# Kernel optimization log

Measured on AMD Instinct MI355X. Metric: run time of the kernel, lower is better.

Reference implementation:

```python
import jax, jax.numpy as jnp
import numpy as np
import math

B, L, D, H = 2, 2048, 1024, 16
DH = D // H  # 64


def setup_inputs() -> dict:
    key = jax.random.key(0)
    ks = jax.random.split(key, 8)
    s = 1.0 / math.sqrt(D)
    return {
        "query": jax.random.normal(ks[0], (B, L, D), dtype=jnp.float32),
        "key": jax.random.normal(ks[1], (B, L, D), dtype=jnp.float32),
        "value": jax.random.normal(ks[2], (B, L, D), dtype=jnp.float32),
        "attn_mask": jax.random.bernoulli(ks[3], 0.1, (B, L, L)),  # True = masked
        "Wq": jax.random.normal(ks[4], (D, D), dtype=jnp.float32) * s,
        "Wk": jax.random.normal(ks[5], (D, D), dtype=jnp.float32) * s,
        "Wv": jax.random.normal(ks[6], (D, D), dtype=jnp.float32) * s,
        "Wo": jax.random.normal(ks[7], (D, D), dtype=jnp.float32) * s,
    }


def reference(query, key, value, attn_mask, Wq, Wk, Wv, Wo):
    # torch nn.Linear computes x @ W.T (bias=False here)
    def shape(x):
        b, l, _ = x.shape
        return x.reshape(b, l, H, DH).transpose(0, 2, 1, 3)  # [B,H,L,DH]

    q = shape(query @ Wq.T) / jnp.sqrt(jnp.float32(DH))
    k = shape(key @ Wk.T)
    v = shape(value @ Wv.T)

    scores = jnp.einsum("bhqd,bhkd->bhqk", q, k)  # [B,H,Q,K]
    if attn_mask is not None:
        scores = jnp.where(attn_mask[:, None, :, :], jnp.float32(-1e18), scores)
    attn = jax.nn.softmax(scores, axis=-1)
    # dropout p=0.0 (eval/deterministic) -> identity
    context = jnp.einsum("bhqk,bhkd->bhqd", attn, v)
    context = context.transpose(0, 2, 1, 3).reshape(query.shape[0], -1, D)
    output = context @ Wo.T
    top_attn = attn[:, 0, :, :]
    return output, top_attn
```

## Files before the change

### kernel.cpp

```cpp
#include <hip/hip_runtime.h>

#define BB 2
#define LL 2048
#define DD 1024
#define HH 16
#define DHH 64

typedef _Float16 f16;
typedef _Float16 f16x8 __attribute__((ext_vector_type(8)));
typedef _Float16 f16x4 __attribute__((ext_vector_type(4)));
typedef _Float16 f16x2 __attribute__((ext_vector_type(2)));
typedef float f32x4 __attribute__((ext_vector_type(4)));
typedef unsigned long long u64;

#define VWAIT(N) asm volatile("s_waitcnt vmcnt(" #N ")" ::: "memory")
#define LWAIT0() asm volatile("s_waitcnt lgkmcnt(0)" ::: "memory")
#define SB0() __builtin_amdgcn_sched_barrier(0)

__device__ __forceinline__ void gload_lds16(const void* g, void* l) {
    __builtin_amdgcn_global_load_lds(
        (const __attribute__((address_space(1))) void*)g,
        (__attribute__((address_space(3))) void*)l, 16, 0, 0);
}

__device__ __forceinline__ f16x4 cvt4f(float4 v) {
    f16x4 o;
    o[0] = (f16)v.x; o[1] = (f16)v.y; o[2] = (f16)v.z; o[3] = (f16)v.w;
    return o;
}

__device__ __forceinline__ f16x8 cvt8f(float4 a, float4 b) {
    f16x2 p0 = __builtin_bit_cast(f16x2, __builtin_amdgcn_cvt_pkrtz(a.x, a.y));
    f16x2 p1 = __builtin_bit_cast(f16x2, __builtin_amdgcn_cvt_pkrtz(a.z, a.w));
    f16x2 p2 = __builtin_bit_cast(f16x2, __builtin_amdgcn_cvt_pkrtz(b.x, b.y));
    f16x2 p3 = __builtin_bit_cast(f16x2, __builtin_amdgcn_cvt_pkrtz(b.z, b.w));
    f16x8 r;
    r[0] = p0[0]; r[1] = p0[1]; r[2] = p1[0]; r[3] = p1[1];
    r[4] = p2[0]; r[5] = p2[1]; r[6] = p3[0]; r[7] = p3[1];
    return r;
}

__global__ void prep(const int* __restrict__ msk,
                     const float* __restrict__ wq, const float* __restrict__ wk,
                     const float* __restrict__ wv, const float* __restrict__ wo,
                     f16* __restrict__ wh, u64* __restrict__ Mp) {
    const int tid = threadIdx.x;
    if (blockIdx.y == 0) {
        const int lane = tid & 63;
        int w = (blockIdx.x * 256 + tid) >> 6;
        const int nw = (1024 * 256) >> 6;
        for (; w < BB * LL * 32; w += nw) {
            int mv = msk[(size_t)w * 64 + lane];
            u64 bits = __ballot(mv != 0);
            if (lane == 0) {
                const int kt = w & 31;
                const int bq = w >> 5;
                const int qq = bq & 2047, b = bq >> 11;
                Mp[((size_t)b * 32 + kt) * LL + qq] = bits;
            }
        }
    } else {
        int i = blockIdx.x * 256 + tid;
        const int stride = 1024 * 256;
        for (; i < 4 * 262144; i += stride) {
            const int sel = i >> 18, j = i & 262143;
            const float* s = sel == 0 ? wq : sel == 1 ? wk : sel == 2 ? wv : wo;
            ((f16x4*)wh)[i] = cvt4f(((const float4*)s)[j]);
        }
    }
}

__global__ void cvt_kernel(const float* __restrict__ src, f16* __restrict__ dst, int n4, float sc) {
    int i = blockIdx.x * blockDim.x + threadIdx.x;
    const int stride = gridDim.x * blockDim.x;
    for (; i < n4; i += stride) {
        float4 v = ((const float4*)src)[i];
        v.x *= sc; v.y *= sc; v.z *= sc; v.w *= sc;
        ((f16x4*)dst)[i] = cvt4f(v);
    }
}
__global__ void cvt4_kernel(const float* __restrict__ a, const float* __restrict__ b,
                            const float* __restrict__ c, const float* __restrict__ d,
                            f16* __restrict__ dst, int n4) {
    const float* s = blockIdx.y == 0 ? a : blockIdx.y == 1 ? b : blockIdx.y == 2 ? c : d;
    f16* o = dst + (size_t)blockIdx.y * n4 * 4;
    int i = blockIdx.x * blockDim.x + threadIdx.x;
    const int stride = gridDim.x * blockDim.x;
    for (; i < n4; i += stride)
        ((f16x4*)o)[i] = cvt4f(((const float4*)s)[i]);
}
__global__ void pack_mask(const int* __restrict__ mask, u64* __restrict__ out, int nwords) {
    const int lane = threadIdx.x & 63;
    int w = (blockIdx.x * blockDim.x + threadIdx.x) >> 6;
    const int nw = (gridDim.x * blockDim.x) >> 6;
    for (; w < nwords; w += nw) {
        int mv = mask[(size_t)w * 64 + lane];
        u64 bits = __ballot(mv != 0);
        if (lane == 0) {
            const int kt = w & 31;
            const int bq = w >> 5;
            const int qq = bq & 2047, b = bq >> 11;
            out[((size_t)b * 32 + kt) * LL + qq] = bits;
        }
    }
}

__global__ __launch_bounds__(256) void gemm_qkv(
        const float* __restrict__ A0, const float* __restrict__ A1, const float* __restrict__ A2,
        const f16* __restrict__ W0, const f16* __restrict__ W1, const f16* __restrict__ W2,
        f16* __restrict__ C0, f16* __restrict__ C1, f16* __restrict__ C2, float scq) {
    __shared__ __align__(16) char lds[49152];
    const int bid = blockIdx.x;
    const int xcd = bid & 7, j = bid >> 3;
    const int p = xcd * 12 + (j >> 3);
    const int xb = j & 7;
    const int z = p >> 5, yb = p & 31;
    const float* __restrict__ A = z == 0 ? A0 : z == 1 ? A1 : A2;
    const f16* __restrict__ W = z == 0 ? W0 : z == 1 ? W1 : W2;
    f16* __restrict__ C       = z == 0 ? C0 : z == 1 ? C1 : C2;

    const int tid = threadIdx.x, wid = tid >> 6, lane = tid & 63;
    const int m0 = yb * 128, n0 = xb * 128;
    const int lq = lane & 15, lg = lane >> 4;
    const int wm = (wid >> 1) << 6, wn = (wid & 1) << 6;
    const int ar0 = (wid * 2) * 16 + (lane >> 2);
    const int ar1 = (wid * 2 + 1) * 16 + (lane >> 2);
    const int ac8 = lane & 3;
    const float* a0p = A + (size_t)(m0 + ar0) * DD + ac8 * 8;
    const float* a1p = A + (size_t)(m0 + ar1) * DD + ac8 * 8;
    char* aw0 = lds + ar0 * 64 + ac8 * 16;
    char* aw1 = lds + ar1 * 64 + ac8 * 16;

    f32x4 acc[4][4] = {};
    float4 arA[2][2], arB[2][2];

    {
        float4 t00 = *(const float4*)(a0p + 0 * 32);
        float4 t01 = *(const float4*)(a0p + 0 * 32 + 4);
        float4 t10 = *(const float4*)(a1p + 0 * 32);
        float4 t11 = *(const float4*)(a1p + 0 * 32 + 4);
        VWAIT(0);
        *(f16x8*)(aw0 + 0 * 8192) = cvt8f(t00, t01);
        *(f16x8*)(aw1 + 0 * 8192) = cvt8f(t10, t11);
        t00 = *(const float4*)(a0p + 1 * 32);
        t01 = *(const float4*)(a0p + 1 * 32 + 4);
        t10 = *(const float4*)(a1p + 1 * 32);
        t11 = *(const float4*)(a1p + 1 * 32 + 4);
        VWAIT(0);
        *(f16x8*)(aw0 + 1 * 8192) = cvt8f(t00, t01);
        *(f16x8*)(aw1 + 1 * 8192) = cvt8f(t10, t11);
        SB0();
        arA[0][0] = *(const float4*)(a0p + 2 * 32);
        arA[0][1] = *(const float4*)(a0p + 2 * 32 + 4);
        arA[1][0] = *(const float4*)(a1p + 2 * 32);
        arA[1][1] = *(const float4*)(a1p + 2 * 32 + 4);
        SB0();
        #pragma unroll
        for (int t = 0; t < 2; ++t)
            #pragma unroll
            for (int jj = 0; jj < 2; ++jj) {
                const int ldsoff = (wid * 2 + jj) << 10;
                const int o = ldsoff + lane * 16;
                const int row = o >> 6, c8 = (o >> 4) & 3;
                gload_lds16(W + (size_t)(n0 + row) * DD + t * 32 + c8 * 8,
                            lds + 24576 + t * 8192 + ldsoff);
            }
        LWAIT0();
    }

    #pragma unroll
    for (int kt = 0; kt < 32; ++kt) {
        VWAIT(2);
        SB0();
        __builtin_amdgcn_s_barrier();
        SB0();
        {
            const int wb = (kt + 2) % 3;
            const int nk = (kt + 3 < 32) ? kt + 3 : 31;
            if ((kt & 1) == 0) {
                *(f16x8*)(aw0 + wb * 8192) = cvt8f(arA[0][0], arA[0][1]);
                *(f16x8*)(aw1 + wb * 8192) = cvt8f(arA[1][0], arA[1][1]);
                SB0();
                arB[0][0] = *(const float4*)(a0p + nk * 32);
                arB[0][1] = *(const float4*)(a0p + nk * 32 + 4);
                arB[1][0] = *(const float4*)(a1p + nk * 32);
                arB[1][1] = *(const float4*)(a1p + nk * 32 + 4);
            } else {
                *(f16x8*)(aw0 + wb * 8192) = cvt8f(arB[0][0], arB[0][1]);
                *(f16x8*)(aw1 + wb * 8192) = cvt8f(arB[1][0], arB[1][1]);
                SB0();
                arA[0][0] = *(const float4*)(a0p + nk * 32);
                arA[0][1] = *(const float4*)(a0p + nk * 32 + 4);
                arA[1][0] = *(const float4*)(a1p + nk * 32);
                arA[1][1] = *(const float4*)(a1p + nk * 32 + 4);
            }
        }
        SB0();
        {
            const int nk = (kt + 2 < 32) ? kt + 2 : 31;
            const int nb = (kt + 2) % 3;
            #pragma unroll
            for (int jj = 0; jj < 2; ++jj) {
                const int ldsoff = (wid * 2 + jj) << 10;
                const int o = ldsoff + lane * 16;
                const int row = o >> 6, c8 = (o >> 4) & 3;
                gload_lds16(W + (size_t)(n0 + row) * DD + nk * 32 + c8 * 8,
                            lds + 24576 + nb * 8192 + ldsoff);
            }
        }
        SB0();

        const int cb = kt % 3;
        const char* Ab = lds + cb * 8192;
        const char* Bb = lds + 24576 + cb * 8192;
        f16x8 af[4], bf[4];
        #pragma unroll
        for (int m = 0; m < 4; ++m)
            af[m] = *(const f16x8*)(Ab + (wm + m * 16 + lq) * 64 + lg * 16);
        #pragma unroll
        for (int n = 0; n < 4; ++n)
            bf[n] = *(const f16x8*)(Bb + (wn + n * 16 + lq) * 64 + lg * 16);
        __builtin_amdgcn_s_setprio(1);
        #pragma unroll
        for (int m = 0; m < 4; ++m)
            #pragma unroll
            for (int n = 0; n < 4; ++n)
                acc[m][n] = __builtin_amdgcn_mfma_f32_16x16x32_f16(af[m], bf[n], acc[m][n], 0, 0, 0);
        __builtin_amdgcn_s_setprio(0);
    }

    const float oscale = (z == 0) ? scq : 1.0f;
    #pragma unroll
    for (int m = 0; m < 4; ++m)
        #pragma unroll
        for (int n = 0; n < 4; ++n)
            #pragma unroll
            for (int r = 0; r < 4; ++r) {
                const int row = m0 + wm + m * 16 + lg * 4 + r;
                const int col = n0 + wn + n * 16 + lq;
                const float val = acc[m][n][r] * oscale;
                if (z < 2) {
                    C[(size_t)row * DD + col] = (f16)val;
                } else {
                    const int b = row >> 11, l = row & 2047;
                    const int h = col >> 6, dh = col & 63;
                    C[((size_t)((b * HH + h) * DHH + dh) << 11) + l] = (f16)val;
                }
            }
}

__global__ __launch_bounds__(256) void gemm_one(const f16* __restrict__ A, const f16* __restrict__ W,
                                                f16* __restrict__ C, int z) {
    __shared__ __align__(16) char lds[49152];
    const int tid = threadIdx.x, wid = tid >> 6, lane = tid & 63;
    const int m0 = blockIdx.y * 128, n0 = blockIdx.x * 128;
    const int lq = lane & 15, lg = lane >> 4;
    const int wm = (wid >> 1) << 6, wn = (wid & 1) << 6;
    f32x4 acc[4][4] = {};

    #pragma unroll
    for (int t = 0; t < 2; ++t)
        #pragma unroll
        for (int jj = 0; jj < 2; ++jj) {
            const int ldsoff = (wid * 2 + jj) << 10;
            const int o = ldsoff + lane * 16;
            const int row = o >> 6, c8 = (o >> 4) & 3;
            gload_lds16(A + (size_t)(m0 + row) * DD + t * 32 + c8 * 8, lds + t * 8192 + ldsoff);
            gload_lds16(W + (size_t)(n0 + row) * DD + t * 32 + c8 * 8, lds + 24576 + t * 8192 + ldsoff);
        }

    for (int kt = 0; kt < 32; ++kt) {
        VWAIT(4);
        SB0();
        __builtin_amdgcn_s_barrier();
        SB0();
        {
            const int nk = (kt + 2 < 32) ? kt + 2 : 31;
            const int nb = (kt + 2) % 3;
            #pragma unroll
            for (int jj = 0; jj < 2; ++jj) {
                const int ldsoff = (wid * 2 + jj) << 10;
                const int o = ldsoff + lane * 16;
                const int row = o >> 6, c8 = (o >> 4) & 3;
                gload_lds16(A + (size_t)(m0 + row) * DD + nk * 32 + c8 * 8,
                            lds + nb * 8192 + ldsoff);
                gload_lds16(W + (size_t)(n0 + row) * DD + nk * 32 + c8 * 8,
                            lds + 24576 + nb * 8192 + ldsoff);
            }
        }
        SB0();

        const int cb = kt % 3;
        const char* Ab = lds + cb * 8192;
        const char* Bb = lds + 24576 + cb * 8192;
        f16x8 af[4], bf[4];
        #pragma unroll
        for (int m = 0; m < 4; ++m)
            af[m] = *(const f16x8*)(Ab + (wm + m * 16 + lq) * 64 + lg * 16);
        #pragma unroll
        for (int n = 0; n < 4; ++n)
            bf[n] = *(const f16x8*)(Bb + (wn + n * 16 + lq) * 64 + lg * 16);
        __builtin_amdgcn_s_setprio(1);
        #pragma unroll
        for (int m = 0; m < 4; ++m)
            #pragma unroll
            for (int n = 0; n < 4; ++n)
                acc[m][n] = __builtin_amdgcn_mfma_f32_16x16x32_f16(af[m], bf[n], acc[m][n], 0, 0, 0);
        __builtin_amdgcn_s_setprio(0);
    }

    #pragma unroll
    for (int m = 0; m < 4; ++m)
        #pragma unroll
        for (int n = 0; n < 4; ++n)
            #pragma unroll
            for (int r = 0; r < 4; ++r) {
                const int row = m0 + wm + m * 16 + lg * 4 + r;
                const int col = n0 + wn + n * 16 + lq;
                const float val = acc[m][n][r];
                if (z < 2) {
                    C[(size_t)row * DD + col] = (f16)val;
                } else {
                    const int b = row >> 11, l = row & 2047;
                    const int h = col >> 6, dh = col & 63;
                    C[((size_t)((b * HH + h) * DHH + dh) << 11) + l] = (f16)val;
                }
            }
}

template<bool TOPF16>
__global__ __launch_bounds__(256) void finale(const f16* __restrict__ A, const f16* __restrict__ W,
                                              float* __restrict__ C, float* __restrict__ top,
                                              const void* __restrict__ src,
                                              const float* __restrict__ linvp) {
    __shared__ __align__(16) char lds[36864];
    const int tid = threadIdx.x;
    if (blockIdx.x >= 512) {
        int i = (blockIdx.x - 512) * 256 + tid;
        const int stride = 1024 * 256;
        if (TOPF16) {
            const f16x8* s8 = (const f16x8*)src;
            const int n = (int)((size_t)BB * LL * LL / 8);
            for (; i < n; i += stride) {
                f16x8 v = s8[i];
                const float linv = linvp[(i * 8) >> 11];
                float4 a, bq;
                a.x = (float)v[0] * linv; a.y = (float)v[1] * linv;
                a.z = (float)v[2] * linv; a.w = (float)v[3] * linv;
                bq.x = (float)v[4] * linv; bq.y = (float)v[5] * linv;
                bq.z = (float)v[6] * linv; bq.w = (float)v[7] * linv;
                ((float4*)top)[i * 2] = a;
                ((float4*)top)[i * 2 + 1] = bq;
            }
        } else {
            const int n = (int)((size_t)BB * LL * LL / 4);
            for (; i < n; i += stride) {
                float4 v = ((const float4*)top)[i];
                const float linv = linvp[(i * 4) >> 11];
                v.x = __builtin_amdgcn_exp2f(v.x) * linv;
                v.y = __builtin_amdgcn_exp2f(v.y) * linv;
                v.z = __builtin_amdgcn_exp2f(v.z) * linv;
                v.w = __builtin_amdgcn_exp2f(v.w) * linv;
                ((float4*)top)[i] = v;
            }
        }
        return;
    }
    const int bid = blockIdx.x;
    const int xcd = bid & 7, j = bid >> 3;
    const int yb = xcd * 4 + (j >> 4);
    const int xb = j & 15;
    const int wid = tid >> 6, lane = tid & 63;
    const int m0 = yb * 128, n0 = xb * 64;
    const int lq = lane & 15, lg = lane >> 4;
    const int wm = wid * 32;
    f32x4 acc[2][4] = {};

    #pragma unroll
    for (int t = 0; t < 2; ++t) {
        #pragma unroll
        for (int j2 = 0; j2 < 2; ++j2) {
            const int o = (j2 * 256 + tid) * 16;
            const int row = o >> 6, c8 = (o >> 4) & 3;
            gload_lds16(A + (size_t)(m0 + row) * DD + t * 32 + c8 * 8,
                        lds + t * 8192 + j2 * 4096 + (wid << 10));
        }
        {
            const int o = tid * 16;
            const int row = o >> 6, c8 = (o >> 4) & 3;
            gload_lds16(W + (size_t)(n0 + row) * DD + t * 32 + c8 * 8,
                        lds + 24576 + t * 4096 + (wid << 10));
        }
    }

    for (int kt = 0; kt < 32; ++kt) {
        VWAIT(3);
        SB0();
        __builtin_amdgcn_s_barrier();
        SB0();
        {
            const int nk = (kt + 2 < 32) ? kt + 2 : 31;
            const int nb = (kt + 2) % 3;
            #pragma unroll
            for (int j2 = 0; j2 < 2; ++j2) {
                const int o = (j2 * 256 + tid) * 16;
                const int row = o >> 6, c8 = (o >> 4) & 3;
                gload_lds16(A + (size_t)(m0 + row) * DD + nk * 32 + c8 * 8,
                            lds + nb * 8192 + j2 * 4096 + (wid << 10));
            }
            {
                const int o = tid * 16;
                const int row = o >> 6, c8 = (o >> 4) & 3;
                gload_lds16(W + (size_t)(n0 + row) * DD + nk * 32 + c8 * 8,
                            lds + 24576 + nb * 4096 + (wid << 10));
            }
        }
        SB0();

        const int cb = kt % 3;
        const char* Ab = lds + cb * 8192;
        const char* Bb = lds + 24576 + cb * 4096;
        f16x8 af[2], bf[4];
        #pragma unroll
        for (int m = 0; m < 2; ++m)
            af[m] = *(const f16x8*)(Ab + (wm + m * 16 + lq) * 64 + lg * 16);
        #pragma unroll
        for (int n = 0; n < 4; ++n)
            bf[n] = *(const f16x8*)(Bb + (n * 16 + lq) * 64 + lg * 16);
        __builtin_amdgcn_s_setprio(1);
        #pragma unroll
        for (int m = 0; m < 2; ++m)
            #pragma unroll
            for (int n = 0; n < 4; ++n)
                acc[m][n] = __builtin_amdgcn_mfma_f32_16x16x32_f16(af[m], bf[n], acc[m][n], 0, 0, 0);
        __builtin_amdgcn_s_setprio(0);
    }

    #pragma unroll
    for (int m = 0; m < 2; ++m)
        #pragma unroll
        for (int n = 0; n < 4; ++n)
            #pragma unroll
            for (int r = 0; r < 4; ++r) {
                const int row = m0 + wm + m * 16 + lg * 4 + r;
                const int col = n0 + n * 16 + lq;
                C[(size_t)row * DD + col] = acc[m][n][r];
            }
}

template<bool TOPF16>
__global__ __launch_bounds__(256) void attn_fwd(const f16* __restrict__ Qp, const f16* __restrict__ Kp,
                                                const f16* __restrict__ VTp,
                                                const u64* __restrict__ Mp,
                                                f16* __restrict__ Op, void* __restrict__ topout,
                                                float* __restrict__ statsLinv) {
    extern __shared__ char lds[];
    const int tid = threadIdx.x, wid = tid >> 6, lane = tid & 63;
    const int lq = lane & 15, lg = lane >> 4;
    const int bid = blockIdx.x;
    const int xcd = bid & 7, j = bid >> 3;
    const int bh = xcd * 4 + (j >> 5);
    const int qt = j & 31;
    const int b = bh >> 4, h = bh & 15;
    const bool topblk = (h == 0);
    const int qrow = qt * 64 + wid * 16 + lq;

    f16x8 qf[2];
    #pragma unroll
    for (int kk = 0; kk < 2; ++kk)
        qf[kk] = *(const f16x8*)(Qp + (size_t)(b * LL + qrow) * DD + h * 64 + (kk * 4 + lg) * 8);

    {
        #pragma unroll
        for (int jj = 0; jj < 2; ++jj) {
            const int o = (wid * 2 + jj) * 1024 + lane * 16;
            const int row = o >> 7, sc = ((o >> 4) & 7) ^ (row & 7);
            gload_lds16(Kp + (size_t)(b * LL + row) * DD + h * 64 + sc * 8,
                        lds + 8192 + (wid * 2 + jj) * 1024);
            gload_lds16(VTp + (size_t)((b * HH + h) * DHH + row) * LL + sc * 8,
                        lds + 24576 + (wid * 2 + jj) * 1024);
        }
    }

    float lsum = 0.f;
    f32x4 acc[4] = {};

    for (int kt = 0; kt < 32; ++kt) {
        if (topblk && kt > 0) { VWAIT(4); } else { VWAIT(0); }
        SB0();
        __builtin_amdgcn_s_barrier();
        SB0();
        const u64 cm = Mp[((size_t)b * 32 + kt) * LL + qrow];
        SB0();
        {
            const int nk = (kt + 1 < 32) ? kt + 1 : 31;
            const int nb = (kt + 1) & 1;
            #pragma unroll
            for (int jj = 0; jj < 2; ++jj) {
                const int o = (wid * 2 + jj) * 1024 + lane * 16;
                const int row = o >> 7, sc = ((o >> 4) & 7) ^ (row & 7);
                gload_lds16(Kp + (size_t)(b * LL + nk * 64 + row) * DD + h * 64 + sc * 8,
                            lds + 8192 + nb * 8192 + (wid * 2 + jj) * 1024);
                gload_lds16(VTp + (size_t)((b * HH + h) * DHH + row) * LL + nk * 64 + sc * 8,
                            lds + 24576 + nb * 8192 + (wid * 2 + jj) * 1024);
            }
        }
        SB0();

        const int cb = kt & 1;
        const char* Kb = lds + 8192 + cb * 8192;
        const char* Vb = lds + 24576 + cb * 8192;

        f32x4 s[4] = {};
        __builtin_amdgcn_s_setprio(1);
        #pragma unroll
        for (int f = 0; f < 4; ++f)
            #pragma unroll
            for (int kk = 0; kk < 2; ++kk) {
                const int co = (((kk * 4 + lg) ^ (lq & 7)) << 4);
                f16x8 kf = *(const f16x8*)(Kb + (f * 16 + lq) * 128 + co);
                s[f] = __builtin_amdgcn_mfma_f32_16x16x32_f16(kf, qf[kk], s[f], 0, 0, 0);
            }
        __builtin_amdgcn_s_setprio(0);

        const u64 wsh = cm >> (lg * 4);
        const unsigned lo = (unsigned)wsh, hi = (unsigned)(wsh >> 32);
        f16x4 ph[4];
        #pragma unroll
        for (int f = 0; f < 4; ++f) {
            const unsigned nib = ((f < 2) ? (lo >> (f * 16)) : (hi >> ((f - 2) * 16))) & 0xFu;
            #pragma unroll
            for (int r = 0; r < 4; ++r)
                if (nib & (1u << r)) s[f][r] = -1e18f;
            const float p0 = __builtin_amdgcn_exp2f(s[f][0]);
            const float p1 = __builtin_amdgcn_exp2f(s[f][1]);
            const float p2 = __builtin_amdgcn_exp2f(s[f][2]);
            const float p3 = __builtin_amdgcn_exp2f(s[f][3]);
            lsum += (p0 + p1) + (p2 + p3);
            f16x2 pa = __builtin_bit_cast(f16x2, __builtin_amdgcn_cvt_pkrtz(p0, p1));
            f16x2 pb = __builtin_bit_cast(f16x2, __builtin_amdgcn_cvt_pkrtz(p2, p3));
            ph[f][0] = pa[0]; ph[f][1] = pa[1]; ph[f][2] = pb[0]; ph[f][3] = pb[1];
        }

        if (topblk) {
            if (TOPF16) {
                f16* T = (f16*)topout;
                #pragma unroll
                for (int f = 0; f < 4; ++f)
                    *(f16x4*)(T + ((size_t)b * LL + qrow) * LL + kt * 64 + f * 16 + lg * 4) = ph[f];
            } else {
                float* T = (float*)topout;
                #pragma unroll
                for (int f = 0; f < 4; ++f)
                    *(f32x4*)(T + ((size_t)b * LL + qrow) * LL + kt * 64 + f * 16 + lg * 4) = s[f];
            }
        }

        #pragma unroll
        for (int f = 0; f < 4; ++f) {
            const int chunk = f * 2 + (lg >> 1);
            const int bo = ((chunk ^ (lq & 7)) << 4) + (lg & 1) * 8;
            *(f16x4*)(lds + (wid << 11) + lq * 128 + bo) = ph[f];
        }

        __builtin_amdgcn_s_setprio(1);
        #pragma unroll
        for (int kk = 0; kk < 2; ++kk) {
            const int co = (((kk * 4 + lg) ^ (lq & 7)) << 4);
            f16x8 pf = *(const f16x8*)(lds + (wid << 11) + lq * 128 + co);
            #pragma unroll
            for (int f = 0; f < 4; ++f) {
                f16x8 vf = *(const f16x8*)(Vb + (f * 16 + lq) * 128 + co);
                acc[f] = __builtin_amdgcn_mfma_f32_16x16x32_f16(vf, pf, acc[f], 0, 0, 0);
            }
        }
        __builtin_amdgcn_s_setprio(0);
    }

    lsum += __shfl_xor(lsum, 16);
    lsum += __shfl_xor(lsum, 32);
    const float linv = 1.f / lsum;
    #pragma unroll
    for (int f = 0; f < 4; ++f) {
        f16x4 ov;
        #pragma unroll
        for (int r = 0; r < 4; ++r) ov[r] = (f16)(acc[f][r] * linv);
        *(f16x4*)(Op + (size_t)(b * LL + qrow) * DD + h * 64 + f * 16 + lg * 4) = ov;
    }
    if (topblk && lg == 0) statsLinv[(size_t)b * LL + qrow] = linv;
}

extern "C" void kernel_launch(void* const* d_in, const int* in_sizes, int n_in,
                              void* d_out, int out_size, void* d_ws, size_t ws_size,
                              hipStream_t stream) {
    const float* q   = (const float*)d_in[0];
    const float* k   = (const float*)d_in[1];
    const float* v   = (const float*)d_in[2];
    const int*   msk = (const int*)d_in[3];
    const float* wq  = (const float*)d_in[4];
    const float* wk  = (const float*)d_in[5];
    const float* wv  = (const float*)d_in[6];
    const float* wo  = (const float*)d_in[7];
    float* out = (float*)d_out;

    const size_t NX = (size_t)BB * LL * DD;
    const size_t NW = (size_t)DD * DD;
    const int NMW = BB * LL * (LL / 64);
    const size_t NXo = NX;
    const float SCQ = 0.125f * 1.4426950408889634f;
    const int ALDS = 40960;

    f16* ws = (f16*)d_ws;
    const size_t needed = (6 * NX + 4 * NW) * 2 + (size_t)NMW * 8 + (size_t)BB * LL * 4;
    const bool fused = ws_size >= needed;

    if (fused) {
        f16* Op   = ws;
        f16* wh   = Op + NX;
        f16* wqh = wh, *wkh = wh + NW, *wvh = wh + 2 * NW, *woh = wh + 3 * NW;
        f16* Qp  = wh + 4 * NW;
        f16* Kp  = Qp + NX;
        f16* VTp = Kp + NX;
        f16* topP = VTp + NX;
        u64* Mp  = (u64*)(topP + 2 * NX);
        float* statsLinv = (float*)(Mp + NMW);

        prep<<<dim3(1024, 2), 256, 0, stream>>>(msk, wq, wk, wv, wo, wh, Mp);
        gemm_qkv<<<768, 256, 0, stream>>>(q, k, v, wqh, wkh, wvh, Qp, Kp, VTp, SCQ);
        attn_fwd<true><<<1024, 256, ALDS, stream>>>(Qp, Kp, VTp, Mp, Op, topP, statsLinv);
        finale<true><<<1536, 256, 0, stream>>>(Op, woh, out, out + NXo, topP, statsLinv);
    } else {
        f16* bufA = ws;
        f16* wh   = bufA + NX;
        f16* wqh = wh, *wkh = wh + NW, *wvh = wh + 2 * NW, *woh = wh + 3 * NW;
        f16* Qp  = wh + 4 * NW;
        f16* Kp  = Qp + NX;
        f16* VTp = Kp + NX;
        u64* Mp  = (u64*)(VTp + NX);
        float* statsLinv = (float*)(Mp + NMW);

        pack_mask<<<256, 256, 0, stream>>>(msk, Mp, NMW);
        cvt4_kernel<<<dim3(128, 4), 256, 0, stream>>>(wq, wk, wv, wo, wh, (int)(NW / 4));
        cvt_kernel<<<2048, 256, 0, stream>>>(q, bufA, (int)(NX / 4), SCQ);
        gemm_one<<<dim3(8, 32), 256, 0, stream>>>(bufA, wqh, Qp, 0);
        cvt_kernel<<<2048, 256, 0, stream>>>(k, bufA, (int)(NX / 4), 1.f);
        gemm_one<<<dim3(8, 32), 256, 0, stream>>>(bufA, wkh, Kp, 1);
        cvt_kernel<<<2048, 256, 0, stream>>>(v, bufA, (int)(NX / 4), 1.f);
        gemm_one<<<dim3(8, 32), 256, 0, stream>>>(bufA, wvh, VTp, 2);
        attn_fwd<false><<<1024, 256, ALDS, stream>>>(Qp, Kp, VTp, Mp, bufA,
                                                     out + NXo, statsLinv);
        finale<false><<<1536, 256, 0, stream>>>(bufA, woh, out, out + NXo, out + NXo, statsLinv);
    }
}
```

Before: 155.4 us.

## Move mask packing into QKV GEMM launch to overlap with GEMM blocks

Splits the prep kernel so it only converts weights, and folds mask bit-packing into the QKV GEMM kernel as 128 extra leading blocks. The packing loop is unrolled four ways so each wave has four loads in flight. The aim is to overlap the memory-bound mask read with the compute-bound GEMM and shorten the prep kernel. The extra blocks shift the GEMM block-to-XCD mapping and hold LDS-sized blocks that do no GEMM work.

```diff
diff --git a/kernel.cpp b/kernel.cpp
--- a/kernel.cpp
+++ b/kernel.cpp
@@ -40,33 +40,15 @@
     return r;
 }
 
-__global__ void prep(const int* __restrict__ msk,
-                     const float* __restrict__ wq, const float* __restrict__ wk,
-                     const float* __restrict__ wv, const float* __restrict__ wo,
-                     f16* __restrict__ wh, u64* __restrict__ Mp) {
-    const int tid = threadIdx.x;
-    if (blockIdx.y == 0) {
-        const int lane = tid & 63;
-        int w = (blockIdx.x * 256 + tid) >> 6;
-        const int nw = (1024 * 256) >> 6;
-        for (; w < BB * LL * 32; w += nw) {
-            int mv = msk[(size_t)w * 64 + lane];
-            u64 bits = __ballot(mv != 0);
-            if (lane == 0) {
-                const int kt = w & 31;
-                const int bq = w >> 5;
-                const int qq = bq & 2047, b = bq >> 11;
-                Mp[((size_t)b * 32 + kt) * LL + qq] = bits;
-            }
-        }
-    } else {
-        int i = blockIdx.x * 256 + tid;
-        const int stride = 1024 * 256;
-        for (; i < 4 * 262144; i += stride) {
-            const int sel = i >> 18, j = i & 262143;
-            const float* s = sel == 0 ? wq : sel == 1 ? wk : sel == 2 ? wv : wo;
-            ((f16x4*)wh)[i] = cvt4f(((const float4*)s)[j]);
-        }
+__global__ void prep_w(const float* __restrict__ wq, const float* __restrict__ wk,
+                       const float* __restrict__ wv, const float* __restrict__ wo,
+                       f16* __restrict__ wh) {
+    int i = blockIdx.x * 256 + threadIdx.x;
+    const int stride = 1024 * 256;
+    for (; i < 4 * 262144; i += stride) {
+        const int sel = i >> 18, j = i & 262143;
+        const float* s = sel == 0 ? wq : sel == 1 ? wk : sel == 2 ? wv : wo;
+        ((f16x4*)wh)[i] = cvt4f(((const float4*)s)[j]);
     }
 }
 
@@ -108,9 +90,35 @@
 __global__ __launch_bounds__(256) void gemm_qkv(
         const float* __restrict__ A0, const float* __restrict__ A1, const float* __restrict__ A2,
         const f16* __restrict__ W0, const f16* __restrict__ W1, const f16* __restrict__ W2,
-        f16* __restrict__ C0, f16* __restrict__ C1, f16* __restrict__ C2, float scq) {
+        f16* __restrict__ C0, f16* __restrict__ C1, f16* __restrict__ C2, float scq,
+        const int* __restrict__ msk, u64* __restrict__ Mp) {
     __shared__ __align__(16) char lds[49152];
-    const int bid = blockIdx.x;
+    const int tid = threadIdx.x;
+    if (blockIdx.x < 128) {
+        const int lane = tid & 63;
+        const int wave = (blockIdx.x * 256 + tid) >> 6;
+        const int nw = 512;
+        for (int w0 = wave; w0 < BB * LL * 32; w0 += 4 * nw) {
+            const int w1 = w0 + nw, w2 = w0 + 2 * nw, w3 = w0 + 3 * nw;
+            const int mv0 = msk[(size_t)w0 * 64 + lane];
+            const int mv1 = msk[(size_t)w1 * 64 + lane];
+            const int mv2 = msk[(size_t)w2 * 64 + lane];
+            const int mv3 = msk[(size_t)w3 * 64 + lane];
+            const u64 b0 = __ballot(mv0 != 0);
+            const u64 b1 = __ballot(mv1 != 0);
+            const u64 b2 = __ballot(mv2 != 0);
+            const u64 b3 = __ballot(mv3 != 0);
+            if (lane == 0) {
+                #define STW(W, B) { const int kt = (W) & 31; const int bq = (W) >> 5;          \
+                                    const int qq = bq & 2047, bb = bq >> 11;                   \
+                                    Mp[((size_t)bb * 32 + kt) * LL + qq] = (B); }
+                STW(w0, b0); STW(w1, b1); STW(w2, b2); STW(w3, b3);
+                #undef STW
+            }
+        }
+        return;
+    }
+    const int bid = blockIdx.x - 128;
     const int xcd = bid & 7, j = bid >> 3;
     const int p = xcd * 12 + (j >> 3);
     const int xb = j & 7;
@@ -119,7 +127,7 @@
     const f16* __restrict__ W = z == 0 ? W0 : z == 1 ? W1 : W2;
     f16* __restrict__ C       = z == 0 ? C0 : z == 1 ? C1 : C2;
 
-    const int tid = threadIdx.x, wid = tid >> 6, lane = tid & 63;
+    const int wid = tid >> 6, lane = tid & 63;
     const int m0 = yb * 128, n0 = xb * 128;
     const int lq = lane & 15, lg = lane >> 4;
     const int wm = (wid >> 1) << 6, wn = (wid & 1) << 6;
@@ -625,8 +633,8 @@
         u64* Mp  = (u64*)(topP + 2 * NX);
         float* statsLinv = (float*)(Mp + NMW);
 
-        prep<<<dim3(1024, 2), 256, 0, stream>>>(msk, wq, wk, wv, wo, wh, Mp);
-        gemm_qkv<<<768, 256, 0, stream>>>(q, k, v, wqh, wkh, wvh, Qp, Kp, VTp, SCQ);
+        prep_w<<<1024, 256, 0, stream>>>(wq, wk, wv, wo, wh);
+        gemm_qkv<<<896, 256, 0, stream>>>(q, k, v, wqh, wkh, wvh, Qp, Kp, VTp, SCQ, msk, Mp);
         attn_fwd<true><<<1024, 256, ALDS, stream>>>(Qp, Kp, VTp, Mp, Op, topP, statsLinv);
         finale<true><<<1536, 256, 0, stream>>>(Op, woh, out, out + NXo, topP, statsLinv);
     } else {
```

After: 161.4 us, median of 2. 1.04x slower.
